# Performance work log

Measured on AMD Instinct MI355X. Metric: run time of the kernel, lower is better.

The kernel has to match this reference:

```python
import jax, jax.numpy as jnp
import numpy as np

EPS = 1e-8


def setup_inputs() -> dict:
    key = jax.random.key(0)
    k0, k1, k2, k3 = jax.random.split(key, 4)
    b, cin, cout, h, w, kk, cond = 16, 512, 512, 64, 64, 3, 512
    return {
        "x": jax.random.normal(k0, (b, cin, h, w), jnp.float32),
        "y": jax.random.normal(k1, (b, cond), jnp.float32),
        "w_conv": jax.random.normal(k2, (cout, cin, kk, kk), jnp.float32) * 0.05,
        "w_gamma": jax.random.normal(k3, (cin, cond), jnp.float32) * 0.05,
        "b_gamma": jnp.ones((cin,), jnp.float32),
    }


def reference(x, y, w_conv, w_gamma, b_gamma):
    # fc_gamma: per-sample per-input-channel modulation scale  [b, cin]
    gamma = y @ w_gamma.T + b_gamma
    # modulate: [b, cout, cin, kh, kw]
    weight = w_conv[None, :, :, :, :] * gamma[:, None, :, None, None]
    # demodulate: rsqrt of sum over (cin, kh, kw) per (b, cout)
    d = jax.lax.rsqrt(jnp.sum(weight * weight, axis=(2, 3, 4), keepdims=True) + EPS)
    weight = weight * d

    # per-sample conv (equivalent to groups=b grouped conv), stride 1, same padding
    def conv_one(xi, wi):
        # xi: [cin, h, w], wi: [cout, cin, kh, kw]
        out = jax.lax.conv_general_dilated(
            xi[None], wi, window_strides=(1, 1), padding=[(1, 1), (1, 1)],
            dimension_numbers=("NCHW", "OIHW", "NCHW"))
        return out[0]

    return jax.vmap(conv_one)(x, weight)  # [b, cout, h, w]
```

## Files before the change

kernel.cpp:

```cpp
#include <hip/hip_runtime.h>
#include <stdint.h>

#define NB   16
#define CIN  512
#define COUT 512
#define HH   64
#define WW   64
#define NCOND 512
#define TAPS 9
#define EPSD 1e-8f

typedef short bf16x8 __attribute__((ext_vector_type(8)));
typedef float f32x4 __attribute__((ext_vector_type(4)));

static __device__ __forceinline__ short f2bf(float f) {
  union { float f; uint32_t u; } c;
  c.f = f;
  uint32_t u = c.u;
  uint32_t r = (u + 0x7FFFu + ((u >> 16) & 1u)) >> 16;
  return (short)(uint16_t)r;
}

static __device__ __forceinline__ void gl_lds16(const void* g, void* l) {
  __builtin_amdgcn_global_load_lds(
      (const __attribute__((address_space(1))) void*)g,
      (__attribute__((address_space(3))) void*)l, 16, 0, 0);
}

__global__ __launch_bounds__(512) void k_gamma(const float* __restrict__ y,
                                               const float* __restrict__ w_gamma,
                                               const float* __restrict__ b_gamma,
                                               float* __restrict__ gamma,
                                               float* __restrict__ zbuf) {
  __shared__ float ys[NCOND];
  const int b = blockIdx.x;
  const int i = threadIdx.x;
  if (zbuf && b == 0) { zbuf[i] = 0.f; zbuf[i + 512] = 0.f; }
  ys[i] = y[b * NCOND + i];
  __syncthreads();
  const float4* wg = reinterpret_cast<const float4*>(w_gamma + (size_t)i * NCOND);
  float acc = b_gamma[i];
  for (int c4 = 0; c4 < NCOND / 4; ++c4) {
    float4 w4 = wg[c4];
    acc += w4.x * ys[c4 * 4 + 0] + w4.y * ys[c4 * 4 + 1] +
           w4.z * ys[c4 * 4 + 2] + w4.w * ys[c4 * 4 + 3];
  }
  gamma[b * CIN + i] = acc;
}

__global__ __launch_bounds__(256) void k_prep2(const float* __restrict__ w_conv,
                                               float* __restrict__ s2,
                                               short* __restrict__ W2) {
  __shared__ float ws_s[CIN * TAPS];
  const int o = blockIdx.x;
  const int t = threadIdx.x;
  const float* wsrc = w_conv + (size_t)o * CIN * TAPS;
  for (int idx = t; idx < CIN * TAPS; idx += 256) ws_s[idx] = wsrc[idx];
  __syncthreads();
  for (int i = t; i < CIN; i += 256) {
    float s = 0.f;
#pragma unroll
    for (int tap = 0; tap < TAPS; ++tap) {
      float v = ws_s[i * TAPS + tap];
      s += v * v;
    }
    s2[(size_t)o * CIN + i] = s;
  }
  const int key = (o >> 1) & 3;
  for (int k = t; k < CIN * TAPS; k += 256) {
    int tap = k >> 9;
    int r = k & 511;
    int c = r >> 5, sl = (r >> 3) & 3, j = r & 7;
    W2[((size_t)(c * TAPS + tap) * COUT + o) * 32 + ((sl ^ key) * 8) + j] =
        f2bf(ws_s[r * TAPS + tap]);
  }
}

__global__ __launch_bounds__(256) void k_prep(const float* __restrict__ w_conv,
                                              float* __restrict__ s2,
                                              short* __restrict__ Wr) {
  __shared__ float ws_s[CIN * TAPS];
  const int o = blockIdx.x;
  const int t = threadIdx.x;
  const float* wsrc = w_conv + (size_t)o * CIN * TAPS;
  for (int idx = t; idx < CIN * TAPS; idx += 256) ws_s[idx] = wsrc[idx];
  __syncthreads();
  for (int i = t; i < CIN; i += 256) {
    float s = 0.f;
#pragma unroll
    for (int tap = 0; tap < TAPS; ++tap) {
      float v = ws_s[i * TAPS + tap];
      s += v * v;
    }
    s2[(size_t)o * CIN + i] = s;
  }
  for (int idx = t; idx < CIN * TAPS; idx += 256) {
    int i = idx & (CIN - 1);
    int tap = idx >> 9;
    Wr[((size_t)o * TAPS + tap) * CIN + i] = f2bf(ws_s[i * TAPS + tap]);
  }
}

__global__ __launch_bounds__(512) void k_d(const float* __restrict__ gamma,
                                           const float* __restrict__ s2,
                                           float* __restrict__ dscale) {
  __shared__ float g2[CIN];
  const int b = blockIdx.x;
  const int o = threadIdx.x;
  float g = gamma[b * CIN + o];
  g2[o] = g * g;
  __syncthreads();
  const float4* s4 = reinterpret_cast<const float4*>(s2 + (size_t)o * CIN);
  float acc = 0.f;
  for (int i4 = 0; i4 < CIN / 4; ++i4) {
    float4 v = s4[i4];
    acc += v.x * g2[i4 * 4 + 0] + v.y * g2[i4 * 4 + 1] +
           v.z * g2[i4 * 4 + 2] + v.w * g2[i4 * 4 + 3];
  }
  dscale[b * COUT + o] = rsqrtf(acc + EPSD);
}

__global__ __launch_bounds__(256) void k_xmod2(const float* __restrict__ x,
                                               const float* __restrict__ gamma,
                                               short* __restrict__ xm) {
  __shared__ float tile[64][67];
  __shared__ float gs[CIN];
  const int y = blockIdx.x, b = blockIdx.y;
  const int t = threadIdx.x;
  gs[t] = gamma[b * CIN + t];
  gs[t + 256] = gamma[b * CIN + t + 256];
  __syncthreads();
  const int w = t >> 2, q = t & 3;
  const int sw = (w >> 1) & 3;
  short* dst = xm + (((size_t)b * HH + y) * WW + w) * CIN;
  for (int c0 = 0; c0 < CIN; c0 += 64) {
    {
      int ww_ = t & 63;
      int cb = t >> 6;
      const float* xp = x + (((size_t)(b * CIN + c0 + cb)) * HH + y) * WW + ww_;
#pragma unroll
      for (int p = 0; p < 16; ++p)
        tile[cb + p * 4][ww_] = xp[(size_t)p * 4 * HH * WW];
    }
    __syncthreads();
#pragma unroll
    for (int h = 0; h < 2; ++h) {
      int c_lo = q * 16 + h * 8;
      int chunk = (c0 + c_lo) >> 5;
      int sl = (c_lo >> 3) & 3;
      short tmp[8];
#pragma unroll
      for (int j = 0; j < 8; ++j)
        tmp[j] = f2bf(tile[c_lo + j][w] * gs[c0 + c_lo + j]);
      *reinterpret_cast<bf16x8*>(dst + chunk * 32 + (sl ^ sw) * 8) =
          *reinterpret_cast<const bf16x8*>(tmp);
    }
    __syncthreads();
  }
}

__global__ __launch_bounds__(512, 2) void k_conv8(const short* __restrict__ xm,
                                                  const short* __restrict__ W2,
                                                  const short* __restrict__ zbuf,
                                                  const float* __restrict__ dscale,
                                                  float* __restrict__ out) {
  __shared__ short Xs[2 * 6 * 64 * 32];
  __shared__ float d_s[256];
  __shared__ __align__(16) short zls[64];

  const int orig = blockIdx.x;
  const int wgid = ((orig & 7) << 6) | (orig >> 3);
  const int ot = wgid >> 8;
  const int b  = (wgid >> 4) & 15;
  const int sp = wgid & 15;

  const int t = threadIdx.x, lane = t & 63;
  const int wv = t >> 6;
  const int wr = wv >> 2;
  const int wc = wv & 3;
  const int l15 = lane & 15;
  const int slA = lane >> 4;

  if (t < 256) d_s[t] = dscale[b * COUT + ot * 256 + t];
  if (t < 64) zls[t] = 0;

  const short* xS[3];
#pragma unroll
  for (int i = 0; i < 3; ++i) {
    int idx = t + 512 * i;
    int rb = idx >> 8;
    int w = (idx & 255) >> 2;
    int sl = idx & 3;
    int ysrc = sp * 4 + rb - 1;
    bool rv = (ysrc >= 0) && (ysrc < HH);
    xS[i] = rv ? xm + (((size_t)b * HH + ysrc) * WW + w) * CIN + sl * 8
               : zbuf + sl * 8;
  }

  const int o0 = ot * 256 + wr * 128 + l15;
  const int keyA = (o0 >> 1) & 3;
  const short* aGc = W2 + (size_t)o0 * 32 + ((slA ^ keyA) * 8);

  const int kb0 = slA << 4;
  const char* pbx[3];
#pragma unroll
  for (int dxi = 0; dxi < 3; ++dxi) {
    int lcc = l15 + dxi - 1;
    int key = (lcc >> 1) & 3;
    pbx[dxi] = (const char*)&Xs[0] + lcc * 64 + (kb0 ^ (key << 4));
  }
  const int lc3 = (l15 + 1 > 15) ? 15 : (l15 + 1);
  const char* pbx3 = (const char*)&Xs[0] + lc3 * 64 + (kb0 ^ (((lc3 >> 1) & 3) << 4));
  char* wx0 = (char*)&Xs[0] + t * 16;
  const char* zl = (const char*)&zls[0];
  const bool mL = (l15 == 0);
  const bool mR = (l15 == 15);

  f32x4 acc[8][4];
#pragma unroll
  for (int m = 0; m < 8; ++m)
#pragma unroll
    for (int n = 0; n < 4; ++n)
      acc[m][n] = (f32x4){0.f, 0.f, 0.f, 0.f};

  bf16x8 aA[8], aB[8];

#pragma unroll
  for (int i = 0; i < 3; ++i)
    gl_lds16(xS[i], wx0 + i * 8192);
#pragma unroll
  for (int m = 0; m < 8; ++m)
    aA[m] = *reinterpret_cast<const bf16x8*>(aGc + m * 512);
  asm volatile("s_waitcnt vmcnt(0) lgkmcnt(0)" ::: "memory");
  __builtin_amdgcn_s_barrier();
  asm volatile("" ::: "memory");

#define DO_TAP(tp, CUR, NXT, NXTOFF, STGX, KNV)                               \
  {                                                                           \
    const short* an_ = aGc + (NXTOFF);                                        \
    _Pragma("unroll") for (int m_ = 0; m_ < 8; ++m_)                          \
        NXT[m_] = *reinterpret_cast<const bf16x8*>(an_ + m_ * 512);           \
    if (STGX) {                                                               \
      _Pragma("unroll") for (int i_ = 0; i_ < 3; ++i_)                        \
          gl_lds16(xS[i_] + (KNV), wxw + i_ * 8192);                          \
    }                                                                         \
    __builtin_amdgcn_sched_barrier(0);                                        \
    {                                                                         \
      const int dy_ = (tp) / 3 - 1, dx_ = (tp) % 3 - 1;                       \
      const int rbo_ = (wc + dy_ + 1) * 4096;                                 \
      bf16x8 bfr[4];                                                          \
      const char* qq_ = (dx_ == -1) ? qq0 : ((dx_ == 0) ? qq1 : qq2);         \
      const char* s0_ = (dx_ == -1 && mL) ? (zl - rbo_) : qq_;                \
      const char* s3_ = (dx_ == 1) ? (mR ? (zl - rbo_ - 3072) : qq3) : qq_;   \
      bfr[0] = *reinterpret_cast<const bf16x8*>(s0_ + rbo_);                  \
      bfr[1] = *reinterpret_cast<const bf16x8*>(qq_ + rbo_ + 1024);           \
      bfr[2] = *reinterpret_cast<const bf16x8*>(qq_ + rbo_ + 2048);           \
      bfr[3] = *reinterpret_cast<const bf16x8*>(s3_ + rbo_ + 3072);           \
      __builtin_amdgcn_s_setprio(1);                                          \
      _Pragma("unroll") for (int m_ = 0; m_ < 8; ++m_)                        \
        _Pragma("unroll") for (int n_ = 0; n_ < 4; ++n_)                      \
          acc[m_][n_] = __builtin_amdgcn_mfma_f32_16x16x32_bf16(              \
              CUR[m_], bfr[n_], acc[m_][n_], 0, 0, 0);                        \
      __builtin_amdgcn_s_setprio(0);                                          \
    }                                                                         \
  }

#define CHUNK_TAPS(A0, A1, NX8, KNV)                                          \
  DO_TAP(0, A0, A1, 16384, false, 0)                                          \
  DO_TAP(1, A1, A0, 32768, false, 0)                                          \
  DO_TAP(2, A0, A1, 49152, false, 0)                                          \
  DO_TAP(3, A1, A0, 65536, false, 0)                                          \
  DO_TAP(4, A0, A1, 81920, false, 0)                                          \
  DO_TAP(5, A1, A0, 98304, false, 0)                                          \
  DO_TAP(6, A0, A1, 114688, false, 0)                                         \
  DO_TAP(7, A1, A0, 131072, true, KNV)                                        \
  DO_TAP(8, A0, A1, (NX8), false, 0)                                          \
  __builtin_amdgcn_sched_barrier(0);                                          \
  asm volatile("s_waitcnt vmcnt(8)" ::: "memory");                            \
  __builtin_amdgcn_s_barrier();                                               \
  asm volatile("" ::: "memory");

  for (int c2 = 0; c2 < 8; ++c2) {
    {
      const char* qq0 = pbx[0];
      const char* qq1 = pbx[1];
      const char* qq2 = pbx[2];
      const char* qq3 = pbx3;
      char* wxw = wx0 + 24576;
      const int knv = (2 * c2 + 1) * 32;
      CHUNK_TAPS(aA, aB, 147456, knv)
    }
    aGc += 147456;
    {
      const char* qq0 = pbx[0] + 24576;
      const char* qq1 = pbx[1] + 24576;
      const char* qq2 = pbx[2] + 24576;
      const char* qq3 = pbx3 + 24576;
      char* wxw = wx0;
      const int knv = (c2 < 7) ? (2 * c2 + 2) * 32 : 0;
      const int nx8 = (c2 < 7) ? 147456 : 0;
      CHUNK_TAPS(aB, aA, nx8, knv)
    }
    aGc += 147456;
  }
#undef CHUNK_TAPS
#undef DO_TAP

#pragma unroll
  for (int m = 0; m < 8; ++m) {
#pragma unroll
    for (int n = 0; n < 4; ++n) {
#pragma unroll
      for (int j = 0; j < 4; ++j) {
        int o_l = wr * 128 + m * 16 + (lane >> 4) * 4 + j;
        int o = ot * 256 + o_l;
        int yy = sp * 4 + wc;
        int cx = n * 16 + l15;
        out[(((size_t)b * COUT + o) * HH + yy) * WW + cx] = d_s[o_l] * acc[m][n][j];
      }
    }
  }
}

__global__ __launch_bounds__(256) void k_conv_fb(const float* __restrict__ x,
                                                 const short* __restrict__ Wr,
                                                 const float* __restrict__ gamma,
                                                 const float* __restrict__ dscale,
                                                 float* __restrict__ out) {
  __shared__ short As[128 * 64];
  __shared__ short Xs[4 * 64 * 64];
  __shared__ float gam_s[CIN];
  __shared__ float d_s[128];

  const int sp = blockIdx.x;
  const int ot = blockIdx.y;
  const int b  = blockIdx.z;
  const int t  = threadIdx.x;
  const int lane = t & 63;
  const int wv = t >> 6;
  const int wr = wv >> 1;
  const int wc = wv & 1;

  gam_s[t] = gamma[b * CIN + t];
  gam_s[t + 256] = gamma[b * CIN + t + 256];
  if (t < 128) d_s[t] = dscale[b * COUT + ot * 128 + t];

  f32x4 acc[4][4];
#pragma unroll
  for (int m = 0; m < 4; ++m)
#pragma unroll
    for (int n = 0; n < 4; ++n)
      acc[m][n] = (f32x4){0.f, 0.f, 0.f, 0.f};

  const int srow = t >> 6;
  const int sc = t & 63;
  const int ysrc = sp * 2 + srow - 1;
  const bool rv = (ysrc >= 0) && (ysrc < HH);
  const int ycl = rv ? ysrc : 0;
  const float* xrow = x + (((size_t)b * CIN) * HH + ycl) * WW + sc;
  short* xs_base = &Xs[(srow * 64 + sc) * 64];
  const int xs_sw = (sc & 7) << 4;

  for (int chunk = 0; chunk < CIN / 64; ++chunk) {
    const int i0 = chunk * 64;
    __syncthreads();
    {
      const float* xp = xrow + (size_t)i0 * (HH * WW);
#pragma unroll
      for (int i8 = 0; i8 < 8; ++i8) {
        short tmp[8];
#pragma unroll
        for (int j = 0; j < 8; ++j) {
          int i = i8 * 8 + j;
          float v = rv ? xp[i * (HH * WW)] : 0.0f;
          tmp[j] = f2bf(v * gam_s[i0 + i]);
        }
        char* dst = (char*)xs_base + ((i8 * 16) ^ xs_sw);
        *reinterpret_cast<bf16x8*>(dst) = *reinterpret_cast<const bf16x8*>(tmp);
      }
    }
    for (int tap = 0; tap < TAPS; ++tap) {
      __syncthreads();
#pragma unroll
      for (int j = 0; j < 4; ++j) {
        int s = t + 256 * j;
        int row = s >> 3, sl = s & 7;
        int kbyte = (sl * 16) ^ ((row & 7) << 4);
        const short* src = Wr + ((size_t)(ot * 128 + row) * TAPS + tap) * CIN +
                           i0 + (kbyte >> 1);
        *reinterpret_cast<bf16x8*>((char*)As + row * 128 + sl * 16) =
            *reinterpret_cast<const bf16x8*>(src);
      }
      __syncthreads();

      const int dy = tap / 3 - 1, dx = tap % 3 - 1;
      bf16x8 afr[2][4], bfr[2][4];
#pragma unroll
      for (int kk = 0; kk < 2; ++kk) {
        const int kb = kk * 64 + (lane >> 4) * 16;
#pragma unroll
        for (int m = 0; m < 4; ++m) {
          int row = wr * 64 + m * 16 + (lane & 15);
          afr[kk][m] = *reinterpret_cast<const bf16x8*>(
              (const char*)As + row * 128 + (kb ^ ((row & 7) << 4)));
        }
#pragma unroll
        for (int n = 0; n < 4; ++n) {
          int p = wc * 64 + n * 16 + (lane & 15);
          int r = p >> 6, c = p & 63;
          int cc = c + dx;
          bool val = (cc >= 0) && (cc < WW);
          int ccl = val ? cc : 0;
          int rr = r + dy + 1;
          bf16x8 f = *reinterpret_cast<const bf16x8*>(
              (const char*)Xs + (rr * 64 + ccl) * 128 + (kb ^ ((ccl & 7) << 4)));
          if (!val) f = (bf16x8){0, 0, 0, 0, 0, 0, 0, 0};
          bfr[kk][n] = f;
        }
      }
#pragma unroll
      for (int m = 0; m < 4; ++m)
#pragma unroll
        for (int n = 0; n < 4; ++n)
#pragma unroll
          for (int kk = 0; kk < 2; ++kk)
            acc[m][n] = __builtin_amdgcn_mfma_f32_16x16x32_bf16(
                afr[kk][m], bfr[kk][n], acc[m][n], 0, 0, 0);
    }
  }

#pragma unroll
  for (int m = 0; m < 4; ++m) {
#pragma unroll
    for (int n = 0; n < 4; ++n) {
#pragma unroll
      for (int j = 0; j < 4; ++j) {
        int o_l = wr * 64 + m * 16 + (lane >> 4) * 4 + j;
        int o = ot * 128 + o_l;
        int p = wc * 64 + n * 16 + (lane & 15);
        int yy = sp * 2 + (p >> 6);
        int cx = p & 63;
        out[(((size_t)b * COUT + o) * HH + yy) * WW + cx] = d_s[o_l] * acc[m][n][j];
      }
    }
  }
}

extern "C" void kernel_launch(void* const* d_in, const int* in_sizes, int n_in,
                              void* d_out, int out_size, void* d_ws, size_t ws_size,
                              hipStream_t stream) {
  const float* x = (const float*)d_in[0];
  const float* y = (const float*)d_in[1];
  const float* w_conv = (const float*)d_in[2];
  const float* w_gamma = (const float*)d_in[3];
  const float* b_gamma = (const float*)d_in[4];
  float* out = (float*)d_out;

  char* ws = (char*)d_ws;
  short* W2 = (short*)ws;
  float* gamma = (float*)(ws + 4849664);
  float* dsc = (float*)(ws + 4882432);
  float* s2 = (float*)(ws + 4915200);
  char* zbuf = ws + 5963776;
  short* xm = (short*)(ws + 5967872);
  const size_t NEED = 5967872 + (size_t)NB * HH * WW * CIN * 2 + 4096;

  const bool fast = ws_size >= NEED;

  if (fast) {
    hipLaunchKernelGGL(k_gamma, dim3(NB), dim3(512), 0, stream, y, w_gamma,
                       b_gamma, gamma, (float*)zbuf);
    hipLaunchKernelGGL(k_prep2, dim3(COUT), dim3(256), 0, stream, w_conv, s2, W2);
    hipLaunchKernelGGL(k_d, dim3(NB), dim3(512), 0, stream, gamma, s2, dsc);
    hipLaunchKernelGGL(k_xmod2, dim3(HH, NB), dim3(256), 0, stream, x, gamma, xm);
    hipLaunchKernelGGL(k_conv8, dim3(512), dim3(512), 0, stream, xm, W2,
                       (const short*)zbuf, dsc, out);
  } else {
    hipLaunchKernelGGL(k_gamma, dim3(NB), dim3(512), 0, stream, y, w_gamma,
                       b_gamma, gamma, (float*)nullptr);
    hipLaunchKernelGGL(k_prep, dim3(COUT), dim3(256), 0, stream, w_conv, s2, W2);
    hipLaunchKernelGGL(k_d, dim3(NB), dim3(512), 0, stream, gamma, s2, dsc);
    hipLaunchKernelGGL(k_conv_fb, dim3(32, 4, NB), dim3(256), 0, stream, x, W2,
                       gamma, dsc, out);
  }
}
```

Before: 335.8 us.

## Switch conv inner loop from 16x16x32 to 32x32x16 bf16 MFMA tiles

Rewrites the main implicit-GEMM conv kernel to use 32x32x16 MFMA instructions instead of 16x16x32, remapping weight fragment loads, LDS pixel addressing (XOR swizzle halves), edge zero-padding handling, and the output write layout. Larger MFMA tiles reduce the number of instructions issued and the LDS fragment reads per FLOP. The cost is a more complex fragment layout, 16-wide accumulators with the same register footprint, and a risk of LDS bank conflicts or layout errors in the swizzle.

```diff
diff --git a/kernel.cpp b/kernel.cpp
--- a/kernel.cpp
+++ b/kernel.cpp
@@ -12,6 +12,7 @@
 
 typedef short bf16x8 __attribute__((ext_vector_type(8)));
 typedef float f32x4 __attribute__((ext_vector_type(4)));
+typedef float f32x16 __attribute__((ext_vector_type(16)));
 
 static __device__ __forceinline__ short f2bf(float f) {
   union { float f; uint32_t u; } c;
@@ -159,14 +160,14 @@
   }
 }
 
-__global__ __launch_bounds__(512, 2) void k_conv8(const short* __restrict__ xm,
+__global__ __launch_bounds__(512, 2) void k_conv9(const short* __restrict__ xm,
                                                   const short* __restrict__ W2,
                                                   const short* __restrict__ zbuf,
                                                   const float* __restrict__ dscale,
                                                   float* __restrict__ out) {
   __shared__ short Xs[2 * 6 * 64 * 32];
   __shared__ float d_s[256];
-  __shared__ __align__(16) short zls[64];
+  __shared__ __align__(64) short zls[64];
 
   const int orig = blockIdx.x;
   const int wgid = ((orig & 7) << 6) | (orig >> 3);
@@ -178,8 +179,8 @@
   const int wv = t >> 6;
   const int wr = wv >> 2;
   const int wc = wv & 3;
-  const int l15 = lane & 15;
-  const int slA = lane >> 4;
+  const int l31 = lane & 31;
+  const int k8 = lane >> 5;
 
   if (t < 256) d_s[t] = dscale[b * COUT + ot * 256 + t];
   if (t < 64) zls[t] = 0;
@@ -197,31 +198,34 @@
                : zbuf + sl * 8;
   }
 
-  const int o0 = ot * 256 + wr * 128 + l15;
-  const int keyA = (o0 >> 1) & 3;
-  const short* aGc = W2 + (size_t)o0 * 32 + ((slA ^ keyA) * 8);
-
-  const int kb0 = slA << 4;
-  const char* pbx[3];
-#pragma unroll
-  for (int dxi = 0; dxi < 3; ++dxi) {
-    int lcc = l15 + dxi - 1;
-    int key = (lcc >> 1) & 3;
-    pbx[dxi] = (const char*)&Xs[0] + lcc * 64 + (kb0 ^ (key << 4));
-  }
-  const int lc3 = (l15 + 1 > 15) ? 15 : (l15 + 1);
-  const char* pbx3 = (const char*)&Xs[0] + lc3 * 64 + (kb0 ^ (((lc3 >> 1) & 3) << 4));
+  const int oL = ot * 256 + wr * 128 + l31;
+  const int key0 = (oL >> 1) & 3;
+  const short* aC0 = W2 + (size_t)oL * 32 + (((0 * 2 + k8) ^ key0) * 8);
+  const short* aC1 = W2 + (size_t)oL * 32 + (((1 * 2 + k8) ^ key0) * 8);
+
+  const char* pb[2][3];
+#pragma unroll
+  for (int nt = 0; nt < 2; ++nt) {
+#pragma unroll
+    for (int dxi = 0; dxi < 3; ++dxi) {
+      int w = nt * 32 + l31 + dxi - 1;
+      int kw = (w >> 1) & 3;
+      pb[nt][dxi] = (const char*)&Xs[0] + w * 64 + ((k8 ^ kw) << 4);
+    }
+  }
   char* wx0 = (char*)&Xs[0] + t * 16;
   const char* zl = (const char*)&zls[0];
-  const bool mL = (l15 == 0);
-  const bool mR = (l15 == 15);
-
-  f32x4 acc[8][4];
-#pragma unroll
-  for (int m = 0; m < 8; ++m)
-#pragma unroll
-    for (int n = 0; n < 4; ++n)
-      acc[m][n] = (f32x4){0.f, 0.f, 0.f, 0.f};
+  const bool mL = (l31 == 0);
+  const bool mR = (l31 == 31);
+
+  f32x16 acc[4][2];
+#pragma unroll
+  for (int mt = 0; mt < 4; ++mt)
+#pragma unroll
+    for (int nt = 0; nt < 2; ++nt)
+#pragma unroll
+      for (int r = 0; r < 16; ++r)
+        acc[mt][nt][r] = 0.f;
 
   bf16x8 aA[8], aB[8];
 
@@ -229,17 +233,23 @@
   for (int i = 0; i < 3; ++i)
     gl_lds16(xS[i], wx0 + i * 8192);
 #pragma unroll
-  for (int m = 0; m < 8; ++m)
-    aA[m] = *reinterpret_cast<const bf16x8*>(aGc + m * 512);
+  for (int mt = 0; mt < 4; ++mt) {
+    aA[mt]     = *reinterpret_cast<const bf16x8*>(aC0 + mt * 1024);
+    aA[4 + mt] = *reinterpret_cast<const bf16x8*>(aC1 + mt * 1024);
+  }
   asm volatile("s_waitcnt vmcnt(0) lgkmcnt(0)" ::: "memory");
   __builtin_amdgcn_s_barrier();
   asm volatile("" ::: "memory");
 
-#define DO_TAP(tp, CUR, NXT, NXTOFF, STGX, KNV)                               \
+#define LD8(p) (*reinterpret_cast<const bf16x8*>(p))
+#define X32(p) ((const char*)(((uintptr_t)(p)) ^ 32))
+
+#define DO_TAP(tp, CUR, NXT, STGX, KNV)                                       \
   {                                                                           \
-    const short* an_ = aGc + (NXTOFF);                                        \
-    _Pragma("unroll") for (int m_ = 0; m_ < 8; ++m_)                          \
-        NXT[m_] = *reinterpret_cast<const bf16x8*>(an_ + m_ * 512);           \
+    _Pragma("unroll") for (int mt_ = 0; mt_ < 4; ++mt_) {                     \
+      NXT[mt_]     = LD8(aC0 + ((tp) + 1) * 16384 + mt_ * 1024);              \
+      NXT[4 + mt_] = LD8(aC1 + ((tp) + 1) * 16384 + mt_ * 1024);              \
+    }                                                                         \
     if (STGX) {                                                               \
       _Pragma("unroll") for (int i_ = 0; i_ < 3; ++i_)                        \
           gl_lds16(xS[i_] + (KNV), wxw + i_ * 8192);                          \
@@ -248,33 +258,35 @@
     {                                                                         \
       const int dy_ = (tp) / 3 - 1, dx_ = (tp) % 3 - 1;                       \
       const int rbo_ = (wc + dy_ + 1) * 4096;                                 \
+      const char* s0_ = ((dx_ == -1) && mL) ? (zl - rbo_) : q0[dx_ + 1];      \
+      const char* s1_ = ((dx_ == 1) && mR) ? (zl - rbo_) : q1[dx_ + 1];       \
       bf16x8 bfr[4];                                                          \
-      const char* qq_ = (dx_ == -1) ? qq0 : ((dx_ == 0) ? qq1 : qq2);         \
-      const char* s0_ = (dx_ == -1 && mL) ? (zl - rbo_) : qq_;                \
-      const char* s3_ = (dx_ == 1) ? (mR ? (zl - rbo_ - 3072) : qq3) : qq_;   \
-      bfr[0] = *reinterpret_cast<const bf16x8*>(s0_ + rbo_);                  \
-      bfr[1] = *reinterpret_cast<const bf16x8*>(qq_ + rbo_ + 1024);           \
-      bfr[2] = *reinterpret_cast<const bf16x8*>(qq_ + rbo_ + 2048);           \
-      bfr[3] = *reinterpret_cast<const bf16x8*>(s3_ + rbo_ + 3072);           \
+      bfr[0] = LD8(s0_ + rbo_);                                               \
+      bfr[1] = LD8(X32(s0_ + rbo_));                                          \
+      bfr[2] = LD8(s1_ + rbo_);                                               \
+      bfr[3] = LD8(X32(s1_ + rbo_));                                          \
       __builtin_amdgcn_s_setprio(1);                                          \
-      _Pragma("unroll") for (int m_ = 0; m_ < 8; ++m_)                        \
-        _Pragma("unroll") for (int n_ = 0; n_ < 4; ++n_)                      \
-          acc[m_][n_] = __builtin_amdgcn_mfma_f32_16x16x32_bf16(              \
-              CUR[m_], bfr[n_], acc[m_][n_], 0, 0, 0);                        \
+      _Pragma("unroll") for (int mt_ = 0; mt_ < 4; ++mt_)                     \
+        _Pragma("unroll") for (int nt_ = 0; nt_ < 2; ++nt_) {                 \
+          acc[mt_][nt_] = __builtin_amdgcn_mfma_f32_32x32x16_bf16(            \
+              CUR[mt_], bfr[nt_ * 2], acc[mt_][nt_], 0, 0, 0);                \
+          acc[mt_][nt_] = __builtin_amdgcn_mfma_f32_32x32x16_bf16(            \
+              CUR[4 + mt_], bfr[nt_ * 2 + 1], acc[mt_][nt_], 0, 0, 0);        \
+        }                                                                     \
       __builtin_amdgcn_s_setprio(0);                                          \
     }                                                                         \
   }
 
-#define CHUNK_TAPS(A0, A1, NX8, KNV)                                          \
-  DO_TAP(0, A0, A1, 16384, false, 0)                                          \
-  DO_TAP(1, A1, A0, 32768, false, 0)                                          \
-  DO_TAP(2, A0, A1, 49152, false, 0)                                          \
-  DO_TAP(3, A1, A0, 65536, false, 0)                                          \
-  DO_TAP(4, A0, A1, 81920, false, 0)                                          \
-  DO_TAP(5, A1, A0, 98304, false, 0)                                          \
-  DO_TAP(6, A0, A1, 114688, false, 0)                                         \
-  DO_TAP(7, A1, A0, 131072, true, KNV)                                        \
-  DO_TAP(8, A0, A1, (NX8), false, 0)                                          \
+#define CHUNK_TAPS(A0, A1, KNV)                                               \
+  DO_TAP(0, A0, A1, false, 0)                                                 \
+  DO_TAP(1, A1, A0, false, 0)                                                 \
+  DO_TAP(2, A0, A1, false, 0)                                                 \
+  DO_TAP(3, A1, A0, false, 0)                                                 \
+  DO_TAP(4, A0, A1, false, 0)                                                 \
+  DO_TAP(5, A1, A0, false, 0)                                                 \
+  DO_TAP(6, A0, A1, false, 0)                                                 \
+  DO_TAP(7, A1, A0, true, KNV)                                                \
+  DO_TAP(8, A0, A1, false, 0)                                                 \
   __builtin_amdgcn_sched_barrier(0);                                          \
   asm volatile("s_waitcnt vmcnt(8)" ::: "memory");                            \
   __builtin_amdgcn_s_barrier();                                               \
@@ -282,41 +294,41 @@
 
   for (int c2 = 0; c2 < 8; ++c2) {
     {
-      const char* qq0 = pbx[0];
-      const char* qq1 = pbx[1];
-      const char* qq2 = pbx[2];
-      const char* qq3 = pbx3;
+      const char* q0[3] = {pb[0][0], pb[0][1], pb[0][2]};
+      const char* q1[3] = {pb[1][0], pb[1][1], pb[1][2]};
       char* wxw = wx0 + 24576;
       const int knv = (2 * c2 + 1) * 32;
-      CHUNK_TAPS(aA, aB, 147456, knv)
-    }
-    aGc += 147456;
+      CHUNK_TAPS(aA, aB, knv)
+    }
+    aC0 += 9 * 16384;
+    aC1 += 9 * 16384;
     {
-      const char* qq0 = pbx[0] + 24576;
-      const char* qq1 = pbx[1] + 24576;
-      const char* qq2 = pbx[2] + 24576;
-      const char* qq3 = pbx3 + 24576;
+      const char* q0[3] = {pb[0][0] + 24576, pb[0][1] + 24576, pb[0][2] + 24576};
+      const char* q1[3] = {pb[1][0] + 24576, pb[1][1] + 24576, pb[1][2] + 24576};
       char* wxw = wx0;
       const int knv = (c2 < 7) ? (2 * c2 + 2) * 32 : 0;
-      const int nx8 = (c2 < 7) ? 147456 : 0;
-      CHUNK_TAPS(aB, aA, nx8, knv)
-    }
-    aGc += 147456;
+      CHUNK_TAPS(aB, aA, knv)
+    }
+    aC0 += 9 * 16384;
+    aC1 += 9 * 16384;
   }
 #undef CHUNK_TAPS
 #undef DO_TAP
-
-#pragma unroll
-  for (int m = 0; m < 8; ++m) {
-#pragma unroll
-    for (int n = 0; n < 4; ++n) {
-#pragma unroll
-      for (int j = 0; j < 4; ++j) {
-        int o_l = wr * 128 + m * 16 + (lane >> 4) * 4 + j;
+#undef X32
+#undef LD8
+
+#pragma unroll
+  for (int mt = 0; mt < 4; ++mt) {
+#pragma unroll
+    for (int nt = 0; nt < 2; ++nt) {
+#pragma unroll
+      for (int r = 0; r < 16; ++r) {
+        int row = (r & 3) + 8 * (r >> 2) + 4 * k8;
+        int o_l = wr * 128 + mt * 32 + row;
         int o = ot * 256 + o_l;
         int yy = sp * 4 + wc;
-        int cx = n * 16 + l15;
-        out[(((size_t)b * COUT + o) * HH + yy) * WW + cx] = d_s[o_l] * acc[m][n][j];
+        int px = nt * 32 + l31;
+        out[(((size_t)b * COUT + o) * HH + yy) * WW + px] = d_s[o_l] * acc[mt][nt][r];
       }
     }
   }
@@ -473,7 +485,7 @@
     hipLaunchKernelGGL(k_prep2, dim3(COUT), dim3(256), 0, stream, w_conv, s2, W2);
     hipLaunchKernelGGL(k_d, dim3(NB), dim3(512), 0, stream, gamma, s2, dsc);
     hipLaunchKernelGGL(k_xmod2, dim3(HH, NB), dim3(256), 0, stream, x, gamma, xm);
-    hipLaunchKernelGGL(k_conv8, dim3(512), dim3(512), 0, stream, xm, W2,
+    hipLaunchKernelGGL(k_conv9, dim3(512), dim3(512), 0, stream, xm, W2,
                        (const short*)zbuf, dsc, out);
   } else {
     hipLaunchKernelGGL(k_gamma, dim3(NB), dim3(512), 0, stream, y, w_gamma,
```

Result: slower. 563.7 us (+67.8%).

## Split conv into 256-thread blocks over 128 output channels, parallelize demod

Applied to the files above, without the earlier changes.

The main conv kernel now uses 256-thread workgroups, each covering 128 output channels instead of 256, launched as 1024 blocks instead of 512. Each thread therefore issues twice as many X staging loads. The demodulation scale kernel is rewritten to spread work over 128 blocks, with each output channel's dot product split into 8 segments. Prep kernel order is also swapped. The aim is better occupancy and load balance across CUs, at the cost of loading more X tile data per output channel computed.

```diff
diff --git a/kernel.cpp b/kernel.cpp
--- a/kernel.cpp
+++ b/kernel.cpp
@@ -48,6 +48,38 @@
   gamma[b * CIN + i] = acc;
 }
 
+__global__ __launch_bounds__(512) void k_d3(const float* __restrict__ gamma,
+                                            const float* __restrict__ s2,
+                                            float* __restrict__ dscale) {
+  __shared__ float g2[CIN];
+  __shared__ float red[512];
+  const int b = blockIdx.x >> 3;
+  const int og = blockIdx.x & 7;
+  const int t = threadIdx.x;
+  float g = gamma[b * CIN + t];
+  g2[t] = g * g;
+  __syncthreads();
+  const int o_l = t >> 3, seg = t & 7;
+  const int o = og * 64 + o_l;
+  const float4* s4 = reinterpret_cast<const float4*>(s2 + (size_t)o * CIN + seg * 64);
+  float p = 0.f;
+#pragma unroll
+  for (int c4 = 0; c4 < 16; ++c4) {
+    float4 v = s4[c4];
+    int base = seg * 64 + c4 * 4;
+    p += v.x * g2[base + 0] + v.y * g2[base + 1] +
+         v.z * g2[base + 2] + v.w * g2[base + 3];
+  }
+  red[t] = p;
+  __syncthreads();
+  if (seg == 0) {
+    float s = 0.f;
+#pragma unroll
+    for (int k = 0; k < 8; ++k) s += red[o_l * 8 + k];
+    dscale[b * COUT + o] = rsqrtf(s + EPSD);
+  }
+}
+
 __global__ __launch_bounds__(256) void k_prep2(const float* __restrict__ w_conv,
                                                float* __restrict__ s2,
                                                short* __restrict__ W2) {
@@ -159,35 +191,33 @@
   }
 }
 
-__global__ __launch_bounds__(512, 2) void k_conv8(const short* __restrict__ xm,
-                                                  const short* __restrict__ W2,
-                                                  const short* __restrict__ zbuf,
-                                                  const float* __restrict__ dscale,
-                                                  float* __restrict__ out) {
+__global__ __launch_bounds__(256, 2) void k_conv12(const short* __restrict__ xm,
+                                                   const short* __restrict__ W2,
+                                                   const short* __restrict__ zbuf,
+                                                   const float* __restrict__ dscale,
+                                                   float* __restrict__ out) {
   __shared__ short Xs[2 * 6 * 64 * 32];
-  __shared__ float d_s[256];
+  __shared__ float d_s[128];
   __shared__ __align__(16) short zls[64];
 
   const int orig = blockIdx.x;
-  const int wgid = ((orig & 7) << 6) | (orig >> 3);
+  const int wgid = ((orig & 7) << 7) | (orig >> 3);
   const int ot = wgid >> 8;
   const int b  = (wgid >> 4) & 15;
   const int sp = wgid & 15;
 
   const int t = threadIdx.x, lane = t & 63;
-  const int wv = t >> 6;
-  const int wr = wv >> 2;
-  const int wc = wv & 3;
+  const int wc = t >> 6;
   const int l15 = lane & 15;
   const int slA = lane >> 4;
 
-  if (t < 256) d_s[t] = dscale[b * COUT + ot * 256 + t];
+  if (t < 128) d_s[t] = dscale[b * COUT + ot * 128 + t];
   if (t < 64) zls[t] = 0;
 
-  const short* xS[3];
-#pragma unroll
-  for (int i = 0; i < 3; ++i) {
-    int idx = t + 512 * i;
+  const short* xS[6];
+#pragma unroll
+  for (int i = 0; i < 6; ++i) {
+    int idx = t + 256 * i;
     int rb = idx >> 8;
     int w = (idx & 255) >> 2;
     int sl = idx & 3;
@@ -197,7 +227,7 @@
                : zbuf + sl * 8;
   }
 
-  const int o0 = ot * 256 + wr * 128 + l15;
+  const int o0 = ot * 128 + l15;
   const int keyA = (o0 >> 1) & 3;
   const short* aGc = W2 + (size_t)o0 * 32 + ((slA ^ keyA) * 8);
 
@@ -226,8 +256,8 @@
   bf16x8 aA[8], aB[8];
 
 #pragma unroll
-  for (int i = 0; i < 3; ++i)
-    gl_lds16(xS[i], wx0 + i * 8192);
+  for (int i = 0; i < 6; ++i)
+    gl_lds16(xS[i], wx0 + i * 4096);
 #pragma unroll
   for (int m = 0; m < 8; ++m)
     aA[m] = *reinterpret_cast<const bf16x8*>(aGc + m * 512);
@@ -241,8 +271,8 @@
     _Pragma("unroll") for (int m_ = 0; m_ < 8; ++m_)                          \
         NXT[m_] = *reinterpret_cast<const bf16x8*>(an_ + m_ * 512);           \
     if (STGX) {                                                               \
-      _Pragma("unroll") for (int i_ = 0; i_ < 3; ++i_)                        \
-          gl_lds16(xS[i_] + (KNV), wxw + i_ * 8192);                          \
+      _Pragma("unroll") for (int i_ = 0; i_ < 6; ++i_)                        \
+          gl_lds16(xS[i_] + (KNV), wxw + i_ * 4096);                          \
     }                                                                         \
     __builtin_amdgcn_sched_barrier(0);                                        \
     {                                                                         \
@@ -312,8 +342,8 @@
     for (int n = 0; n < 4; ++n) {
 #pragma unroll
       for (int j = 0; j < 4; ++j) {
-        int o_l = wr * 128 + m * 16 + (lane >> 4) * 4 + j;
-        int o = ot * 256 + o_l;
+        int o_l = m * 16 + (lane >> 4) * 4 + j;
+        int o = ot * 128 + o_l;
         int yy = sp * 4 + wc;
         int cx = n * 16 + l15;
         out[(((size_t)b * COUT + o) * HH + yy) * WW + cx] = d_s[o_l] * acc[m][n][j];
@@ -468,12 +498,12 @@
   const bool fast = ws_size >= NEED;
 
   if (fast) {
+    hipLaunchKernelGGL(k_prep2, dim3(COUT), dim3(256), 0, stream, w_conv, s2, W2);
     hipLaunchKernelGGL(k_gamma, dim3(NB), dim3(512), 0, stream, y, w_gamma,
                        b_gamma, gamma, (float*)zbuf);
-    hipLaunchKernelGGL(k_prep2, dim3(COUT), dim3(256), 0, stream, w_conv, s2, W2);
-    hipLaunchKernelGGL(k_d, dim3(NB), dim3(512), 0, stream, gamma, s2, dsc);
+    hipLaunchKernelGGL(k_d3, dim3(128), dim3(512), 0, stream, gamma, s2, dsc);
     hipLaunchKernelGGL(k_xmod2, dim3(HH, NB), dim3(256), 0, stream, x, gamma, xm);
-    hipLaunchKernelGGL(k_conv8, dim3(512), dim3(512), 0, stream, xm, W2,
+    hipLaunchKernelGGL(k_conv12, dim3(1024), dim3(256), 0, stream, xm, W2,
                        (const short*)zbuf, dsc, out);
   } else {
     hipLaunchKernelGGL(k_gamma, dim3(NB), dim3(512), 0, stream, y, w_gamma,
```

Result: faster. 312.4 us (-7.0%).
